# Performance work log

Measured on AMD Instinct MI355X. Metric: run time of the kernel, lower is better.

The kernel has to match this reference:

```python
import jax, jax.numpy as jnp
import numpy as np

VOCAB_SIZES = [100003, 100019, 100043, 100049, 100057, 100069, 100103, 100109,
               100129, 100151, 100153, 100169, 100183, 100189, 100193, 100207]
OFFSETS = np.cumsum([0] + VOCAB_SIZES[:-1]).astype(np.int32)  # per-head offsets into shared table
B, S, G, C = 2, 2048, 4, 2048        # batch, seq, hc_mult branches, base_emb_dim
H, DH = 16, 64                        # total hash heads, dim_per_head
ENGRAM_DIM = H * DH                   # 1024 = num_orders * dim_per_ngram
K, DIL = 4, 3                         # conv kernel_size, dilation = max_ngram_size


def setup_inputs() -> dict:
  key = jax.random.key(0)
  ks = jax.random.split(key, 8)
  total_vocab = sum(VOCAB_SIZES)
  return {
      "hidden_states": jax.random.normal(ks[0], (B, S, G, C), jnp.float32),
      "hash_input_ids": jax.random.randint(ks[1], (B, S, H), 0, min(VOCAB_SIZES), jnp.int32),
      "emb_table": jax.random.normal(ks[2], (total_vocab, DH), jnp.float32) * 0.02,
      "key_w": jax.random.normal(ks[3], (G, ENGRAM_DIM, C), jnp.float32) / np.sqrt(ENGRAM_DIM),
      "key_b": jnp.zeros((G, C), jnp.float32),
      "k_scale": jnp.ones((G, C), jnp.float32) + 0.02 * jax.random.normal(ks[4], (G, C), jnp.float32),
      "q_scale": jnp.ones((G, C), jnp.float32) + 0.02 * jax.random.normal(ks[5], (G, C), jnp.float32),
      "value_w": jax.random.normal(ks[6], (ENGRAM_DIM, C), jnp.float32) / np.sqrt(ENGRAM_DIM),
      "value_b": jnp.zeros((C,), jnp.float32),
      "conv_scale": jnp.ones((G, C), jnp.float32),
      "conv_w": jax.random.normal(ks[7], (K, G * C), jnp.float32) * 0.25,  # depthwise taps
  }


def _rmsnorm(x, scale, eps):
  var = jnp.mean(jnp.square(x), axis=-1, keepdims=True)
  return x * jax.lax.rsqrt(var + eps) * scale


def reference(hidden_states, hash_input_ids, emb_table, key_w, key_b,
              k_scale, q_scale, value_w, value_b, conv_scale, conv_w):
  # 1. Retrieve: offset-shifted multi-head embedding gather
  ids = hash_input_ids + jnp.asarray(OFFSETS)            # (B,S,H)
  emb = emb_table[ids].reshape(B, S, ENGRAM_DIM)         # (B,S,H*DH)
  # 2. Gate: per-branch key projections + RMSNorms, signed-sqrt sigmoid gate
  keys = jnp.einsum('bse,geo->bsgo', emb, key_w) + key_b  # (B,S,G,C)
  k = _rmsnorm(keys, k_scale, 1e-6)
  q = _rmsnorm(hidden_states, q_scale, 1e-6)
  qk = jnp.einsum('bsgc,bsgc->bsg', q, k) / jnp.sqrt(jnp.float32(C))
  gate_logits = jnp.sqrt(jnp.maximum(jnp.abs(qk), 1e-6)) * jnp.sign(qk)
  gates = jax.nn.sigmoid(gate_logits)                    # (B,S,G)
  value = emb @ value_w + value_b                        # (B,S,C)
  v = gates[..., None] * value[:, :, None, :]            # (B,S,G,C)
  # 3. Mix: ShortConv = SiLU(depthwise causal dilated Conv1D(RMSNorm(v)))
  xn = _rmsnorm(v, conv_scale, 1e-5).reshape(B, S, G * C)
  pad = (K - 1) * DIL                                    # causal left pad = 9
  xp = jnp.pad(xn, ((0, 0), (pad, 0), (0, 0)))
  y = sum(xp[:, j * DIL:j * DIL + S, :] * conv_w[j] for j in range(K))
  y = jax.nn.silu(y).reshape(B, S, G, C)
  return v + y
```

## Files before the change

### kernel.cpp

```cpp
#include <hip/hip_runtime.h>
#include <cstdint>
#include <cstddef>

typedef __attribute__((ext_vector_type(8))) __bf16 bf16x8;
typedef __attribute__((ext_vector_type(4))) float f32x4;
typedef __attribute__((ext_vector_type(4))) unsigned short u16x4;
typedef __attribute__((ext_vector_type(8))) unsigned short u16x8;

static constexpr int Bz = 2, Sz = 2048, Gz = 4, Cz = 2048;
static constexpr int Hh = 16, EDz = 1024;
static constexpr int Tz = Bz * Sz;
static constexpr int NALL = Gz * Cz + Cz;

__constant__ int OFF16[16] = {0, 100003, 200022, 300065, 400114, 500171, 600240,
                              700343, 800452, 900581, 1000732, 1100885, 1201054,
                              1301237, 1401426, 1501619};

__device__ __forceinline__ float bf2f(unsigned short s) {
  union { unsigned u; float f; } x; x.u = ((unsigned)s) << 16; return x.f;
}
__device__ __forceinline__ unsigned short f2bf(float f) {
  union { float f; unsigned u; } x; x.f = f;
  unsigned r = x.u + 0x7fff + ((x.u >> 16) & 1);
  return (unsigned short)(r >> 16);
}

__global__ __launch_bounds__(256) void k_prep0(float* __restrict__ sums) {
  int i = blockIdx.x * 256 + threadIdx.x;
  if (i < 53248) sums[i] = 0.f;
}

__global__ __launch_bounds__(256) void k_prepw(const float* __restrict__ key_w,
                                               const float* __restrict__ value_w,
                                               unsigned short* __restrict__ Wt) {
  __shared__ float tile[32][33];
  const int mat = blockIdx.y;
  const int ot = blockIdx.x & 63, kt = blockIdx.x >> 6;
  const float* src = (mat < 4) ? (key_w + (size_t)mat * EDz * Cz) : value_w;
  const int tx = threadIdx.x & 31, ty = threadIdx.x >> 5;
#pragma unroll
  for (int i = 0; i < 4; i++)
    tile[ty + i * 8][tx] = src[(size_t)(kt * 32 + ty + i * 8) * Cz + ot * 32 + tx];
  __syncthreads();
#pragma unroll
  for (int i = 0; i < 4; i++)
    Wt[(size_t)(mat * Cz + ot * 32 + ty + i * 8) * EDz + kt * 32 + tx] =
        f2bf(tile[tx][ty + i * 8]);
}

__global__ __launch_bounds__(256) void k_gather(const int* __restrict__ ids,
                                                const float* __restrict__ table,
                                                unsigned short* __restrict__ emb) {
  const int t = blockIdx.x;
  const int tid = threadIdx.x;
  const int h = tid >> 4;
  const int d = (tid & 15) * 4;
  const long row = (long)(ids[t * Hh + h] + OFF16[h]);
  f32x4 v = *reinterpret_cast<const f32x4*>(table + row * 64 + d);
  u16x4 o;
#pragma unroll
  for (int i = 0; i < 4; i++) o[i] = f2bf(v[i]);
  *reinterpret_cast<u16x4*>(emb + (size_t)t * EDz + tid * 4) = o;
}

#define GEMM_BAR  asm volatile("s_barrier" ::: "memory")
#define GEMM_V4   asm volatile("s_waitcnt vmcnt(4)" ::: "memory")

__global__ __launch_bounds__(512, 2) void k_gemm8f(const unsigned short* __restrict__ A,
                                                   const unsigned short* __restrict__ Bw,
                                                   const float* __restrict__ hidden,
                                                   const float* __restrict__ key_b,
                                                   const float* __restrict__ value_b,
                                                   const float* __restrict__ q_scale,
                                                   const float* __restrict__ k_scale,
                                                   float* __restrict__ sums,
                                                   unsigned short* __restrict__ vbuf) {
  __shared__ unsigned short s_lds[65536];
  char* lds_c = (char*)s_lds;

  const int tid = threadIdx.x;
  const int wid = tid >> 6, lane = tid & 63;
  const int wr = wid >> 2, wc = wid & 3;

  const int bid = blockIdx.x;
  const int swz = (bid & 7) * 80 + (bid >> 3);
  const int bm = swz / 40, bn = swz % 40;
  const int m0 = bm * 256, n0 = bn * 256;

  int rq[2], kq[2];
#pragma unroll
  for (int q = 0; q < 2; q++) {
    int x = q * 8192 + wid * 1024 + lane * 16;
    int y = x ^ (((x >> 9) & 1) << 5);
    rq[q] = ((y >> 11) & 7) * 16 + ((y >> 6) & 15);
    kq[q] = ((y >> 10) & 1) * 32 + ((y >> 1) & 31);
  }
  const int rdb = (((lane & 15) << 6) + ((lane >> 4) << 4)) ^ (((lane >> 3) & 1) << 5);

  const unsigned short* Arow0 = A + (size_t)m0 * EDz;
  const unsigned short* Arow1 = A + (size_t)(m0 + 128) * EDz;
  const unsigned short* Brow0 = Bw + (size_t)n0 * EDz;
  const unsigned short* Brow1 = Bw + (size_t)(n0 + 128) * EDz;

  auto STAGE = [&](const unsigned short* grow, int ldsOff, int kt) {
#pragma unroll
    for (int q = 0; q < 2; q++) {
      const unsigned short* src = grow + (size_t)rq[q] * EDz + kt * 64 + kq[q];
      __builtin_amdgcn_global_load_lds(
          (const __attribute__((address_space(1))) void*)src,
          (__attribute__((address_space(3))) void*)(lds_c + ldsOff + q * 8192 + wid * 1024),
          16, 0, 0);
    }
  };

  f32x4 acc[8][4] = {};
  bf16x8 Af[4][2], Bl[2][2], Bh[2][2];

  auto RD_A = [&](int buf, int msel) {
    const char* p = lds_c + buf * 32768 + wr * 16384 + rdb;
#pragma unroll
    for (int m = 0; m < 4; m++)
#pragma unroll
      for (int ks = 0; ks < 2; ks++)
        Af[m][ks] = *reinterpret_cast<const bf16x8*>(p + (msel * 4 + m) * 2048 + ks * 1024);
  };
  auto RD_B = [&](int buf, int nsel, bf16x8 (&Bf)[2][2]) {
    const char* p = lds_c + 65536 + buf * 32768 + (wc >> 1) * 16384 + (wc & 1) * 8192 + rdb;
#pragma unroll
    for (int n = 0; n < 2; n++)
#pragma unroll
      for (int ks = 0; ks < 2; ks++)
        Bf[n][ks] = *reinterpret_cast<const bf16x8*>(p + (nsel * 2 + n) * 2048 + ks * 1024);
  };
  auto MM = [&](int msel, int nsel, bf16x8 (&Bf)[2][2]) {
    __builtin_amdgcn_s_setprio(1);
#pragma unroll
    for (int m = 0; m < 4; m++)
#pragma unroll
      for (int n = 0; n < 2; n++)
#pragma unroll
        for (int ks = 0; ks < 2; ks++)
          acc[msel * 4 + m][nsel * 2 + n] = __builtin_amdgcn_mfma_f32_16x16x32_bf16(
              Af[m][ks], Bf[n][ks], acc[msel * 4 + m][nsel * 2 + n], 0, 0, 0);
    __builtin_amdgcn_s_setprio(0);
  };

  STAGE(Arow0, 0,             0);
  STAGE(Arow1, 16384,         0);
  STAGE(Brow0, 65536,         0);
  STAGE(Brow1, 65536 + 16384, 0);
  STAGE(Brow0, 65536 + 32768,         1);
  STAGE(Brow1, 65536 + 32768 + 16384, 1);
  GEMM_V4;
  GEMM_BAR;

  for (int i = 0; i < 8; ++i) {
    const int o  = 2 * i + 1;
    const int t2 = (2 * i + 2 > 15) ? 15 : 2 * i + 2;
    const int t3 = (2 * i + 3 > 15) ? 15 : 2 * i + 3;
    RD_A(0, 0); RD_B(0, 0, Bl);
    STAGE(Arow0, 32768, o);
    GEMM_BAR; MM(0, 0, Bl); GEMM_BAR;
    RD_B(0, 1, Bh);
    STAGE(Arow1, 32768 + 16384, o);
    GEMM_BAR; MM(0, 1, Bh); GEMM_BAR;
    RD_A(0, 1);
    STAGE(Brow0, 65536, t2);
    GEMM_BAR; MM(1, 0, Bl); GEMM_BAR;
    STAGE(Brow1, 65536 + 16384, t2);
    GEMM_V4;
    GEMM_BAR; MM(1, 1, Bh); GEMM_BAR;
    RD_A(1, 0); RD_B(1, 0, Bl);
    STAGE(Arow0, 0, t2);
    GEMM_BAR; MM(0, 0, Bl); GEMM_BAR;
    RD_B(1, 1, Bh);
    STAGE(Arow1, 16384, t2);
    GEMM_BAR; MM(0, 1, Bh); GEMM_BAR;
    RD_A(1, 1);
    STAGE(Brow0, 65536 + 32768, t3);
    GEMM_BAR; MM(1, 0, Bl); GEMM_BAR;
    STAGE(Brow1, 65536 + 32768 + 16384, t3);
    GEMM_V4;
    GEMM_BAR; MM(1, 1, Bh); GEMM_BAR;
  }

  float* sum_q2  = sums;
  float* sum_k2  = sums + 16384;
  float* sum_qwk = sums + 32768;
  float* sum_v2  = sums + 49152;

  if (n0 < 8192) {
    const int g = n0 >> 11;
#pragma unroll
    for (int mrep = 0; mrep < 8; mrep++) {
      const int rowb = wr * 128 + mrep * 16 + (lane >> 4) * 4;
#pragma unroll
      for (int nrep = 0; nrep < 4; nrep++) {
        const int coll = wc * 64 + nrep * 16 + (lane & 15);
        const float kb = key_b[n0 + coll];
#pragma unroll
        for (int t = 0; t < 4; t++) {
          const int row = rowb + t;
          const int addr = (row * 512 + coll * 2) ^ ((row & 15) << 4);
          *reinterpret_cast<unsigned short*>(lds_c + addr) =
              f2bf(acc[mrep][nrep][t] + kb);
        }
      }
    }
    __syncthreads();
    const int wrow = wid * 32;
    const int lrow = lane >> 3;
    const int lsub = lane & 7;
#pragma unroll
    for (int rr = 0; rr < 4; rr++) {
      const int row = wrow + rr * 8 + lrow;
      const int grow = m0 + row;
      const float* hp = hidden + (size_t)grow * 8192 + n0;
      float a_k2 = 0.f, a_qwk = 0.f, a_q2 = 0.f;
#pragma unroll
      for (int c8 = 0; c8 < 4; c8++) {
        const int lc = c8 * 64 + lsub * 8;
        const int addr = (row * 512 + lc * 2) ^ ((row & 15) << 4);
        bf16x8 k8 = *reinterpret_cast<const bf16x8*>(lds_c + addr);
        f32x4 h0 = *reinterpret_cast<const f32x4*>(hp + lc);
        f32x4 h1 = *reinterpret_cast<const f32x4*>(hp + lc + 4);
        f32x4 qs0 = *reinterpret_cast<const f32x4*>(q_scale + n0 + lc);
        f32x4 qs1 = *reinterpret_cast<const f32x4*>(q_scale + n0 + lc + 4);
        f32x4 ks0 = *reinterpret_cast<const f32x4*>(k_scale + n0 + lc);
        f32x4 ks1 = *reinterpret_cast<const f32x4*>(k_scale + n0 + lc + 4);
#pragma unroll
        for (int i = 0; i < 8; i++) {
          const float kf = (float)k8[i];
          const float hf = (i < 4) ? h0[i] : h1[i - 4];
          const float wf = ((i < 4) ? qs0[i] : qs1[i - 4]) *
                           ((i < 4) ? ks0[i] : ks1[i - 4]);
          a_k2  += kf * kf;
          a_qwk += kf * hf * wf;
          a_q2  += hf * hf;
        }
      }
#pragma unroll
      for (int msk = 1; msk <= 4; msk <<= 1) {
        a_k2  += __shfl_xor(a_k2, msk);
        a_qwk += __shfl_xor(a_qwk, msk);
        a_q2  += __shfl_xor(a_q2, msk);
      }
      if (lsub == 0) {
        const int idx = grow * 4 + g;
        atomicAdd(&sum_k2[idx], a_k2);
        atomicAdd(&sum_qwk[idx], a_qwk);
        atomicAdd(&sum_q2[idx], a_q2);
      }
    }
  } else {
#pragma unroll
    for (int mrep = 0; mrep < 8; mrep++) {
      const int rowb = m0 + wr * 128 + mrep * 16 + (lane >> 4) * 4;
      float av2[4] = {0.f, 0.f, 0.f, 0.f};
#pragma unroll
      for (int nrep = 0; nrep < 4; nrep++) {
        const int vcol = n0 - 8192 + wc * 64 + nrep * 16 + (lane & 15);
        const float vb = value_b[vcol];
#pragma unroll
        for (int t = 0; t < 4; t++) {
          const float v = acc[mrep][nrep][t] + vb;
          av2[t] += v * v;
          vbuf[(size_t)(rowb + t) * 2048 + vcol] = f2bf(v);
        }
      }
#pragma unroll
      for (int t = 0; t < 4; t++) {
        float a = av2[t];
#pragma unroll
        for (int msk = 1; msk <= 8; msk <<= 1) a += __shfl_xor(a, msk);
        if ((lane & 15) == 0) atomicAdd(&sum_v2[rowb + t], a);
      }
    }
  }
}

__global__ __launch_bounds__(256) void k_gatefin(const float* __restrict__ sums,
                                                 float* __restrict__ gates,
                                                 float* __restrict__ rstd) {
  const int i = blockIdx.x * 256 + threadIdx.x;
  const float* sum_q2  = sums;
  const float* sum_k2  = sums + 16384;
  const float* sum_qwk = sums + 32768;
  const float* sum_v2  = sums + 49152;
  const int t = i >> 2;
  const float invC = 1.f / 2048.f;
  const float inv_sqrtC = 0.02209708691f;
  float rqv = rsqrtf(sum_q2[i] * invC + 1e-6f);
  float rkv = rsqrtf(sum_k2[i] * invC + 1e-6f);
  float qk = sum_qwk[i] * rqv * rkv * inv_sqrtC;
  float l = sqrtf(fmaxf(fabsf(qk), 1e-6f));
  l = (qk < 0.f) ? -l : l;
  float gate = 1.f / (1.f + expf(-l));
  gates[i] = gate;
  rstd[i] = rsqrtf(gate * gate * (sum_v2[t] * invC) + 1e-5f);
}

__global__ __launch_bounds__(256) void k_conv(const unsigned short* __restrict__ vbuf,
                                              const float* __restrict__ gates,
                                              const float* __restrict__ rstd,
                                              const float* __restrict__ conv_scale,
                                              const float* __restrict__ conv_w,
                                              float* __restrict__ out) {
  const int th = threadIdx.x;
  const int r = blockIdx.x % 3, seg = blockIdx.x / 3;
  const int bg = blockIdx.y;
  const int b = bg >> 2, g = bg & 3;
  const int c8 = th * 8;
  const int ch = g * Cz + c8;

  float cs[8], w0[8], w1[8], w2[8], w3[8];
#pragma unroll
  for (int q = 0; q < 2; q++) {
    f32x4 a = *reinterpret_cast<const f32x4*>(conv_scale + ch + q * 4);
    f32x4 t0 = *reinterpret_cast<const f32x4*>(conv_w + 0 * 8192 + ch + q * 4);
    f32x4 t1 = *reinterpret_cast<const f32x4*>(conv_w + 1 * 8192 + ch + q * 4);
    f32x4 t2 = *reinterpret_cast<const f32x4*>(conv_w + 2 * 8192 + ch + q * 4);
    f32x4 t3 = *reinterpret_cast<const f32x4*>(conv_w + 3 * 8192 + ch + q * 4);
#pragma unroll
    for (int i = 0; i < 4; i++) {
      cs[q * 4 + i] = a[i];
      w0[q * 4 + i] = t0[i]; w1[q * 4 + i] = t1[i];
      w2[q * 4 + i] = t2[i]; w3[q * 4 + i] = t3[i];
    }
  }

  const int s_begin = seg * 64, s_end = s_begin + 64;
  const int s0 = s_begin + ((r - s_begin) % 3 + 3) % 3;

  float p1[8], p2[8], p3[8];
  auto ldxn = [&](int s, float* dst) {
    if (s < 0) {
#pragma unroll
      for (int i = 0; i < 8; i++) dst[i] = 0.f;
      return;
    }
    const int t = b * Sz + s;
    const float grs = gates[t * 4 + g] * rstd[t * 4 + g];
    u16x8 raw = *reinterpret_cast<const u16x8*>(vbuf + (size_t)t * 2048 + c8);
#pragma unroll
    for (int i = 0; i < 8; i++) dst[i] = bf2f(raw[i]) * grs * cs[i];
  };
  ldxn(s0 - 3, p1); ldxn(s0 - 6, p2); ldxn(s0 - 9, p3);

  for (int s = s0; s < s_end; s += 3) {
    const int t = b * Sz + s;
    const float gate = gates[t * 4 + g];
    const float rsc = rstd[t * 4 + g];
    u16x8 raw = *reinterpret_cast<const u16x8*>(vbuf + (size_t)t * 2048 + c8);
    f32x4 o0, o1;
#pragma unroll
    for (int i = 0; i < 8; i++) {
      float v = bf2f(raw[i]) * gate;
      float xn = v * rsc * cs[i];
      float y = w3[i] * xn + w2[i] * p1[i] + w1[i] * p2[i] + w0[i] * p3[i];
      float sy = y / (1.f + expf(-y));
      float ov = v + sy;
      if (i < 4) o0[i] = ov; else o1[i - 4] = ov;
      p3[i] = p2[i]; p2[i] = p1[i]; p1[i] = xn;
    }
    float* op = out + (size_t)t * (Gz * Cz) + ch;
    *reinterpret_cast<f32x4*>(op) = o0;
    *reinterpret_cast<f32x4*>(op + 4) = o1;
  }
}

extern "C" void kernel_launch(void* const* d_in, const int* in_sizes, int n_in,
                              void* d_out, int out_size, void* d_ws, size_t ws_size,
                              hipStream_t stream) {
  const float* hidden     = (const float*)d_in[0];
  const int*   hashids    = (const int*)d_in[1];
  const float* table      = (const float*)d_in[2];
  const float* key_w      = (const float*)d_in[3];
  const float* key_b      = (const float*)d_in[4];
  const float* k_scale    = (const float*)d_in[5];
  const float* q_scale    = (const float*)d_in[6];
  const float* value_w    = (const float*)d_in[7];
  const float* value_b    = (const float*)d_in[8];
  const float* conv_scale = (const float*)d_in[9];
  const float* conv_w     = (const float*)d_in[10];
  float* out = (float*)d_out;
  char* ws = (char*)d_ws;

  unsigned short* emb  = (unsigned short*)(ws + 0);
  unsigned short* Wt   = (unsigned short*)(ws + 8388608);
  unsigned short* vbuf = (unsigned short*)(ws + 29360128);
  float* sums  = (float*)(ws + 46137344);
  float* gates = (float*)(ws + 46350336);
  float* rstd  = (float*)(ws + 46415872);

  k_prep0<<<dim3(208), dim3(256), 0, stream>>>(sums);
  k_prepw<<<dim3(2048, 5), dim3(256), 0, stream>>>(key_w, value_w, Wt);
  k_gather<<<dim3(Tz), dim3(256), 0, stream>>>(hashids, table, emb);
  k_gemm8f<<<dim3(640), dim3(512), 0, stream>>>(emb, Wt, hidden, key_b, value_b,
                                                q_scale, k_scale, sums, vbuf);
  k_gatefin<<<dim3(64), dim3(256), 0, stream>>>(sums, gates, rstd);
  k_conv<<<dim3(96, 8), dim3(256), 0, stream>>>(vbuf, gates, rstd, conv_scale, conv_w, out);
}
```

Before: 202.0 us.

## Halve GEMM N-tile to 128 and double the grid

Shrinks the fused key/value GEMM block tile from 256x256 to 256x128. The B operand is now staged as a single 128-row slab with smaller LDS buffers, the pipeline schedule and vmcnt waits are reworked, and the epilogue swizzle is adjusted. The launch grid doubles to 1280 blocks, which gives finer wave granularity and a smaller tail, plus lower LDS and register pressure. In exchange, arithmetic intensity drops and A tiles are reloaded twice as often.

```diff
diff --git a/kernel.cpp b/kernel.cpp
--- a/kernel.cpp
+++ b/kernel.cpp
@@ -64,7 +64,7 @@
 }
 
 #define GEMM_BAR  asm volatile("s_barrier" ::: "memory")
-#define GEMM_V4   asm volatile("s_waitcnt vmcnt(4)" ::: "memory")
+#define GEMM_V2   asm volatile("s_waitcnt vmcnt(2)" ::: "memory")
 
 __global__ __launch_bounds__(512, 2) void k_gemm8f(const unsigned short* __restrict__ A,
                                                    const unsigned short* __restrict__ Bw,
@@ -75,7 +75,7 @@
                                                    const float* __restrict__ k_scale,
                                                    float* __restrict__ sums,
                                                    unsigned short* __restrict__ vbuf) {
-  __shared__ unsigned short s_lds[65536];
+  __shared__ unsigned short s_lds[49152];
   char* lds_c = (char*)s_lds;
 
   const int tid = threadIdx.x;
@@ -83,9 +83,9 @@
   const int wr = wid >> 2, wc = wid & 3;
 
   const int bid = blockIdx.x;
-  const int swz = (bid & 7) * 80 + (bid >> 3);
-  const int bm = swz / 40, bn = swz % 40;
-  const int m0 = bm * 256, n0 = bn * 256;
+  const int swz = (bid & 7) * 160 + (bid >> 3);
+  const int bm = swz / 80, bn = swz % 80;
+  const int m0 = bm * 256, n0 = bn * 128;
 
   int rq[2], kq[2];
 #pragma unroll
@@ -99,8 +99,7 @@
 
   const unsigned short* Arow0 = A + (size_t)m0 * EDz;
   const unsigned short* Arow1 = A + (size_t)(m0 + 128) * EDz;
-  const unsigned short* Brow0 = Bw + (size_t)n0 * EDz;
-  const unsigned short* Brow1 = Bw + (size_t)(n0 + 128) * EDz;
+  const unsigned short* Brow  = Bw + (size_t)n0 * EDz;
 
   auto STAGE = [&](const unsigned short* grow, int ldsOff, int kt) {
 #pragma unroll
@@ -113,8 +112,8 @@
     }
   };
 
-  f32x4 acc[8][4] = {};
-  bf16x8 Af[4][2], Bl[2][2], Bh[2][2];
+  f32x4 acc[8][2] = {};
+  bf16x8 Af[4][2], Bf[2][2];
 
   auto RD_A = [&](int buf, int msel) {
     const char* p = lds_c + buf * 32768 + wr * 16384 + rdb;
@@ -124,15 +123,15 @@
       for (int ks = 0; ks < 2; ks++)
         Af[m][ks] = *reinterpret_cast<const bf16x8*>(p + (msel * 4 + m) * 2048 + ks * 1024);
   };
-  auto RD_B = [&](int buf, int nsel, bf16x8 (&Bf)[2][2]) {
-    const char* p = lds_c + 65536 + buf * 32768 + (wc >> 1) * 16384 + (wc & 1) * 8192 + rdb;
+  auto RD_B = [&](int buf) {
+    const char* p = lds_c + 65536 + buf * 16384 + rdb;
 #pragma unroll
     for (int n = 0; n < 2; n++)
 #pragma unroll
       for (int ks = 0; ks < 2; ks++)
-        Bf[n][ks] = *reinterpret_cast<const bf16x8*>(p + (nsel * 2 + n) * 2048 + ks * 1024);
-  };
-  auto MM = [&](int msel, int nsel, bf16x8 (&Bf)[2][2]) {
+        Bf[n][ks] = *reinterpret_cast<const bf16x8*>(p + (wc * 2 + n) * 2048 + ks * 1024);
+  };
+  auto MM = [&](int msel) {
     __builtin_amdgcn_s_setprio(1);
 #pragma unroll
     for (int m = 0; m < 4; m++)
@@ -140,48 +139,38 @@
       for (int n = 0; n < 2; n++)
 #pragma unroll
         for (int ks = 0; ks < 2; ks++)
-          acc[msel * 4 + m][nsel * 2 + n] = __builtin_amdgcn_mfma_f32_16x16x32_bf16(
-              Af[m][ks], Bf[n][ks], acc[msel * 4 + m][nsel * 2 + n], 0, 0, 0);
+          acc[msel * 4 + m][n] = __builtin_amdgcn_mfma_f32_16x16x32_bf16(
+              Af[m][ks], Bf[n][ks], acc[msel * 4 + m][n], 0, 0, 0);
     __builtin_amdgcn_s_setprio(0);
   };
 
   STAGE(Arow0, 0,             0);
   STAGE(Arow1, 16384,         0);
-  STAGE(Brow0, 65536,         0);
-  STAGE(Brow1, 65536 + 16384, 0);
-  STAGE(Brow0, 65536 + 32768,         1);
-  STAGE(Brow1, 65536 + 32768 + 16384, 1);
-  GEMM_V4;
+  STAGE(Brow,  65536,         0);
+  STAGE(Brow,  65536 + 16384, 1);
+  GEMM_V2;
   GEMM_BAR;
 
   for (int i = 0; i < 8; ++i) {
     const int o  = 2 * i + 1;
     const int t2 = (2 * i + 2 > 15) ? 15 : 2 * i + 2;
     const int t3 = (2 * i + 3 > 15) ? 15 : 2 * i + 3;
-    RD_A(0, 0); RD_B(0, 0, Bl);
+    RD_A(0, 0); RD_B(0);
     STAGE(Arow0, 32768, o);
-    GEMM_BAR; MM(0, 0, Bl); GEMM_BAR;
-    RD_B(0, 1, Bh);
+    GEMM_BAR; MM(0); GEMM_BAR;
+    RD_A(0, 1);
     STAGE(Arow1, 32768 + 16384, o);
-    GEMM_BAR; MM(0, 1, Bh); GEMM_BAR;
-    RD_A(0, 1);
-    STAGE(Brow0, 65536, t2);
-    GEMM_BAR; MM(1, 0, Bl); GEMM_BAR;
-    STAGE(Brow1, 65536 + 16384, t2);
-    GEMM_V4;
-    GEMM_BAR; MM(1, 1, Bh); GEMM_BAR;
-    RD_A(1, 0); RD_B(1, 0, Bl);
+    STAGE(Brow,  65536, t2);
+    GEMM_V2;
+    GEMM_BAR; MM(1); GEMM_BAR;
+    RD_A(1, 0); RD_B(1);
     STAGE(Arow0, 0, t2);
-    GEMM_BAR; MM(0, 0, Bl); GEMM_BAR;
-    RD_B(1, 1, Bh);
+    GEMM_BAR; MM(0); GEMM_BAR;
+    RD_A(1, 1);
     STAGE(Arow1, 16384, t2);
-    GEMM_BAR; MM(0, 1, Bh); GEMM_BAR;
-    RD_A(1, 1);
-    STAGE(Brow0, 65536 + 32768, t3);
-    GEMM_BAR; MM(1, 0, Bl); GEMM_BAR;
-    STAGE(Brow1, 65536 + 32768 + 16384, t3);
-    GEMM_V4;
-    GEMM_BAR; MM(1, 1, Bh); GEMM_BAR;
+    STAGE(Brow,  65536 + 16384, t3);
+    GEMM_V2;
+    GEMM_BAR; MM(1); GEMM_BAR;
   }
 
   float* sum_q2  = sums;
@@ -195,13 +184,13 @@
     for (int mrep = 0; mrep < 8; mrep++) {
       const int rowb = wr * 128 + mrep * 16 + (lane >> 4) * 4;
 #pragma unroll
-      for (int nrep = 0; nrep < 4; nrep++) {
-        const int coll = wc * 64 + nrep * 16 + (lane & 15);
+      for (int nrep = 0; nrep < 2; nrep++) {
+        const int coll = wc * 32 + nrep * 16 + (lane & 15);
         const float kb = key_b[n0 + coll];
 #pragma unroll
         for (int t = 0; t < 4; t++) {
           const int row = rowb + t;
-          const int addr = (row * 512 + coll * 2) ^ ((row & 15) << 4);
+          const int addr = row * 256 + ((coll * 2) ^ ((row & 7) << 4));
           *reinterpret_cast<unsigned short*>(lds_c + addr) =
               f2bf(acc[mrep][nrep][t] + kb);
         }
@@ -218,9 +207,9 @@
       const float* hp = hidden + (size_t)grow * 8192 + n0;
       float a_k2 = 0.f, a_qwk = 0.f, a_q2 = 0.f;
 #pragma unroll
-      for (int c8 = 0; c8 < 4; c8++) {
+      for (int c8 = 0; c8 < 2; c8++) {
         const int lc = c8 * 64 + lsub * 8;
-        const int addr = (row * 512 + lc * 2) ^ ((row & 15) << 4);
+        const int addr = row * 256 + ((lc * 2) ^ ((row & 7) << 4));
         bf16x8 k8 = *reinterpret_cast<const bf16x8*>(lds_c + addr);
         f32x4 h0 = *reinterpret_cast<const f32x4*>(hp + lc);
         f32x4 h1 = *reinterpret_cast<const f32x4*>(hp + lc + 4);
@@ -258,8 +247,8 @@
       const int rowb = m0 + wr * 128 + mrep * 16 + (lane >> 4) * 4;
       float av2[4] = {0.f, 0.f, 0.f, 0.f};
 #pragma unroll
-      for (int nrep = 0; nrep < 4; nrep++) {
-        const int vcol = n0 - 8192 + wc * 64 + nrep * 16 + (lane & 15);
+      for (int nrep = 0; nrep < 2; nrep++) {
+        const int vcol = n0 - 8192 + wc * 32 + nrep * 16 + (lane & 15);
         const float vb = value_b[vcol];
 #pragma unroll
         for (int t = 0; t < 4; t++) {
@@ -396,8 +385,8 @@
   k_prep0<<<dim3(208), dim3(256), 0, stream>>>(sums);
   k_prepw<<<dim3(2048, 5), dim3(256), 0, stream>>>(key_w, value_w, Wt);
   k_gather<<<dim3(Tz), dim3(256), 0, stream>>>(hashids, table, emb);
-  k_gemm8f<<<dim3(640), dim3(512), 0, stream>>>(emb, Wt, hidden, key_b, value_b,
-                                                q_scale, k_scale, sums, vbuf);
+  k_gemm8f<<<dim3(1280), dim3(512), 0, stream>>>(emb, Wt, hidden, key_b, value_b,
+                                                 q_scale, k_scale, sums, vbuf);
   k_gatefin<<<dim3(64), dim3(256), 0, stream>>>(sums, gates, rstd);
   k_conv<<<dim3(96, 8), dim3(256), 0, stream>>>(vbuf, gates, rstd, conv_scale, conv_w, out);
 }
```

Measured after the change: 232.5 us. 15.1% more time.

## Split value GEMM into narrower 256x128 tiles to balance the block grid

Applied to the files above, without the earlier changes.

The fused key/value GEMM now uses 256x256 tiles only for the key columns (512 blocks). The value projection gets its own path with 256x128 tiles (256 blocks), which has a separate staging schedule, LDS layout and epilogue. This raises the grid from 640 to 768 blocks, aiming to improve wave quantization and load balance across CUs. In exchange the value tiles reuse less data per loaded A tile, and there is more code duplication and register variance between the two branches.

```diff
diff --git a/kernel.cpp b/kernel.cpp
--- a/kernel.cpp
+++ b/kernel.cpp
@@ -65,6 +65,7 @@
 
 #define GEMM_BAR  asm volatile("s_barrier" ::: "memory")
 #define GEMM_V4   asm volatile("s_waitcnt vmcnt(4)" ::: "memory")
+#define GEMM_V2   asm volatile("s_waitcnt vmcnt(2)" ::: "memory")
 
 __global__ __launch_bounds__(512, 2) void k_gemm8f(const unsigned short* __restrict__ A,
                                                    const unsigned short* __restrict__ Bw,
@@ -82,11 +83,6 @@
   const int wid = tid >> 6, lane = tid & 63;
   const int wr = wid >> 2, wc = wid & 3;
 
-  const int bid = blockIdx.x;
-  const int swz = (bid & 7) * 80 + (bid >> 3);
-  const int bm = swz / 40, bn = swz % 40;
-  const int m0 = bm * 256, n0 = bn * 256;
-
   int rq[2], kq[2];
 #pragma unroll
   for (int q = 0; q < 2; q++) {
@@ -97,99 +93,104 @@
   }
   const int rdb = (((lane & 15) << 6) + ((lane >> 4) << 4)) ^ (((lane >> 3) & 1) << 5);
 
-  const unsigned short* Arow0 = A + (size_t)m0 * EDz;
-  const unsigned short* Arow1 = A + (size_t)(m0 + 128) * EDz;
-  const unsigned short* Brow0 = Bw + (size_t)n0 * EDz;
-  const unsigned short* Brow1 = Bw + (size_t)(n0 + 128) * EDz;
-
-  auto STAGE = [&](const unsigned short* grow, int ldsOff, int kt) {
-#pragma unroll
-    for (int q = 0; q < 2; q++) {
-      const unsigned short* src = grow + (size_t)rq[q] * EDz + kt * 64 + kq[q];
-      __builtin_amdgcn_global_load_lds(
-          (const __attribute__((address_space(1))) void*)src,
-          (__attribute__((address_space(3))) void*)(lds_c + ldsOff + q * 8192 + wid * 1024),
-          16, 0, 0);
-    }
-  };
-
-  f32x4 acc[8][4] = {};
-  bf16x8 Af[4][2], Bl[2][2], Bh[2][2];
-
-  auto RD_A = [&](int buf, int msel) {
-    const char* p = lds_c + buf * 32768 + wr * 16384 + rdb;
-#pragma unroll
-    for (int m = 0; m < 4; m++)
-#pragma unroll
-      for (int ks = 0; ks < 2; ks++)
-        Af[m][ks] = *reinterpret_cast<const bf16x8*>(p + (msel * 4 + m) * 2048 + ks * 1024);
-  };
-  auto RD_B = [&](int buf, int nsel, bf16x8 (&Bf)[2][2]) {
-    const char* p = lds_c + 65536 + buf * 32768 + (wc >> 1) * 16384 + (wc & 1) * 8192 + rdb;
-#pragma unroll
-    for (int n = 0; n < 2; n++)
-#pragma unroll
-      for (int ks = 0; ks < 2; ks++)
-        Bf[n][ks] = *reinterpret_cast<const bf16x8*>(p + (nsel * 2 + n) * 2048 + ks * 1024);
-  };
-  auto MM = [&](int msel, int nsel, bf16x8 (&Bf)[2][2]) {
-    __builtin_amdgcn_s_setprio(1);
-#pragma unroll
-    for (int m = 0; m < 4; m++)
-#pragma unroll
-      for (int n = 0; n < 2; n++)
-#pragma unroll
-        for (int ks = 0; ks < 2; ks++)
-          acc[msel * 4 + m][nsel * 2 + n] = __builtin_amdgcn_mfma_f32_16x16x32_bf16(
-              Af[m][ks], Bf[n][ks], acc[msel * 4 + m][nsel * 2 + n], 0, 0, 0);
-    __builtin_amdgcn_s_setprio(0);
-  };
-
-  STAGE(Arow0, 0,             0);
-  STAGE(Arow1, 16384,         0);
-  STAGE(Brow0, 65536,         0);
-  STAGE(Brow1, 65536 + 16384, 0);
-  STAGE(Brow0, 65536 + 32768,         1);
-  STAGE(Brow1, 65536 + 32768 + 16384, 1);
-  GEMM_V4;
-  GEMM_BAR;
-
-  for (int i = 0; i < 8; ++i) {
-    const int o  = 2 * i + 1;
-    const int t2 = (2 * i + 2 > 15) ? 15 : 2 * i + 2;
-    const int t3 = (2 * i + 3 > 15) ? 15 : 2 * i + 3;
-    RD_A(0, 0); RD_B(0, 0, Bl);
-    STAGE(Arow0, 32768, o);
-    GEMM_BAR; MM(0, 0, Bl); GEMM_BAR;
-    RD_B(0, 1, Bh);
-    STAGE(Arow1, 32768 + 16384, o);
-    GEMM_BAR; MM(0, 1, Bh); GEMM_BAR;
-    RD_A(0, 1);
-    STAGE(Brow0, 65536, t2);
-    GEMM_BAR; MM(1, 0, Bl); GEMM_BAR;
-    STAGE(Brow1, 65536 + 16384, t2);
-    GEMM_V4;
-    GEMM_BAR; MM(1, 1, Bh); GEMM_BAR;
-    RD_A(1, 0); RD_B(1, 0, Bl);
-    STAGE(Arow0, 0, t2);
-    GEMM_BAR; MM(0, 0, Bl); GEMM_BAR;
-    RD_B(1, 1, Bh);
-    STAGE(Arow1, 16384, t2);
-    GEMM_BAR; MM(0, 1, Bh); GEMM_BAR;
-    RD_A(1, 1);
-    STAGE(Brow0, 65536 + 32768, t3);
-    GEMM_BAR; MM(1, 0, Bl); GEMM_BAR;
-    STAGE(Brow1, 65536 + 32768 + 16384, t3);
-    GEMM_V4;
-    GEMM_BAR; MM(1, 1, Bh); GEMM_BAR;
-  }
-
   float* sum_q2  = sums;
   float* sum_k2  = sums + 16384;
   float* sum_qwk = sums + 32768;
   float* sum_v2  = sums + 49152;
 
-  if (n0 < 8192) {
+  if (blockIdx.x < 512) {
+    const int bid = blockIdx.x;
+    const int swz = (bid & 7) * 64 + (bid >> 3);
+    const int bm = swz >> 5, bn = swz & 31;
+    const int m0 = bm * 256, n0 = bn * 256;
+
+    const unsigned short* Arow0 = A + (size_t)m0 * EDz;
+    const unsigned short* Arow1 = A + (size_t)(m0 + 128) * EDz;
+    const unsigned short* Brow0 = Bw + (size_t)n0 * EDz;
+    const unsigned short* Brow1 = Bw + (size_t)(n0 + 128) * EDz;
+
+    auto STAGE = [&](const unsigned short* grow, int ldsOff, int kt) {
+#pragma unroll
+      for (int q = 0; q < 2; q++) {
+        const unsigned short* src = grow + (size_t)rq[q] * EDz + kt * 64 + kq[q];
+        __builtin_amdgcn_global_load_lds(
+            (const __attribute__((address_space(1))) void*)src,
+            (__attribute__((address_space(3))) void*)(lds_c + ldsOff + q * 8192 + wid * 1024),
+            16, 0, 0);
+      }
+    };
+
+    f32x4 acc[8][4] = {};
+    bf16x8 Af[4][2], Bl[2][2], Bh[2][2];
+
+    auto RD_A = [&](int buf, int msel) {
+      const char* p = lds_c + buf * 32768 + wr * 16384 + rdb;
+#pragma unroll
+      for (int m = 0; m < 4; m++)
+#pragma unroll
+        for (int ks = 0; ks < 2; ks++)
+          Af[m][ks] = *reinterpret_cast<const bf16x8*>(p + (msel * 4 + m) * 2048 + ks * 1024);
+    };
+    auto RD_B = [&](int buf, int nsel, bf16x8 (&Bf)[2][2]) {
+      const char* p = lds_c + 65536 + buf * 32768 + (wc >> 1) * 16384 + (wc & 1) * 8192 + rdb;
+#pragma unroll
+      for (int n = 0; n < 2; n++)
+#pragma unroll
+        for (int ks = 0; ks < 2; ks++)
+          Bf[n][ks] = *reinterpret_cast<const bf16x8*>(p + (nsel * 2 + n) * 2048 + ks * 1024);
+    };
+    auto MM = [&](int msel, int nsel, bf16x8 (&Bf)[2][2]) {
+      __builtin_amdgcn_s_setprio(1);
+#pragma unroll
+      for (int m = 0; m < 4; m++)
+#pragma unroll
+        for (int n = 0; n < 2; n++)
+#pragma unroll
+          for (int ks = 0; ks < 2; ks++)
+            acc[msel * 4 + m][nsel * 2 + n] = __builtin_amdgcn_mfma_f32_16x16x32_bf16(
+                Af[m][ks], Bf[n][ks], acc[msel * 4 + m][nsel * 2 + n], 0, 0, 0);
+      __builtin_amdgcn_s_setprio(0);
+    };
+
+    STAGE(Arow0, 0,             0);
+    STAGE(Arow1, 16384,         0);
+    STAGE(Brow0, 65536,         0);
+    STAGE(Brow1, 65536 + 16384, 0);
+    STAGE(Brow0, 65536 + 32768,         1);
+    STAGE(Brow1, 65536 + 32768 + 16384, 1);
+    GEMM_V4;
+    GEMM_BAR;
+
+    for (int i = 0; i < 8; ++i) {
+      const int o  = 2 * i + 1;
+      const int t2 = (2 * i + 2 > 15) ? 15 : 2 * i + 2;
+      const int t3 = (2 * i + 3 > 15) ? 15 : 2 * i + 3;
+      RD_A(0, 0); RD_B(0, 0, Bl);
+      STAGE(Arow0, 32768, o);
+      GEMM_BAR; MM(0, 0, Bl); GEMM_BAR;
+      RD_B(0, 1, Bh);
+      STAGE(Arow1, 32768 + 16384, o);
+      GEMM_BAR; MM(0, 1, Bh); GEMM_BAR;
+      RD_A(0, 1);
+      STAGE(Brow0, 65536, t2);
+      GEMM_BAR; MM(1, 0, Bl); GEMM_BAR;
+      STAGE(Brow1, 65536 + 16384, t2);
+      GEMM_V4;
+      GEMM_BAR; MM(1, 1, Bh); GEMM_BAR;
+      RD_A(1, 0); RD_B(1, 0, Bl);
+      STAGE(Arow0, 0, t2);
+      GEMM_BAR; MM(0, 0, Bl); GEMM_BAR;
+      RD_B(1, 1, Bh);
+      STAGE(Arow1, 16384, t2);
+      GEMM_BAR; MM(0, 1, Bh); GEMM_BAR;
+      RD_A(1, 1);
+      STAGE(Brow0, 65536 + 32768, t3);
+      GEMM_BAR; MM(1, 0, Bl); GEMM_BAR;
+      STAGE(Brow1, 65536 + 32768 + 16384, t3);
+      GEMM_V4;
+      GEMM_BAR; MM(1, 1, Bh); GEMM_BAR;
+    }
+
     const int g = n0 >> 11;
 #pragma unroll
     for (int mrep = 0; mrep < 8; mrep++) {
@@ -253,17 +254,98 @@
       }
     }
   } else {
+    const int vb = blockIdx.x - 512;
+    const int swz = (vb & 7) * 32 + (vb >> 3);
+    const int bm = swz >> 4, bn = swz & 15;
+    const int m0 = bm * 256, n0v = bn * 128;
+
+    const unsigned short* Arow0 = A + (size_t)m0 * EDz;
+    const unsigned short* Arow1 = A + (size_t)(m0 + 128) * EDz;
+    const unsigned short* Brow  = Bw + (size_t)(8192 + n0v) * EDz;
+
+    auto STAGE = [&](const unsigned short* grow, int ldsOff, int kt) {
+#pragma unroll
+      for (int q = 0; q < 2; q++) {
+        const unsigned short* src = grow + (size_t)rq[q] * EDz + kt * 64 + kq[q];
+        __builtin_amdgcn_global_load_lds(
+            (const __attribute__((address_space(1))) void*)src,
+            (__attribute__((address_space(3))) void*)(lds_c + ldsOff + q * 8192 + wid * 1024),
+            16, 0, 0);
+      }
+    };
+
+    f32x4 acc[8][2] = {};
+    bf16x8 Af[4][2], Bf[2][2];
+
+    auto RD_A = [&](int buf, int msel) {
+      const char* p = lds_c + buf * 32768 + wr * 16384 + rdb;
+#pragma unroll
+      for (int m = 0; m < 4; m++)
+#pragma unroll
+        for (int ks = 0; ks < 2; ks++)
+          Af[m][ks] = *reinterpret_cast<const bf16x8*>(p + (msel * 4 + m) * 2048 + ks * 1024);
+    };
+    auto RD_B = [&](int buf) {
+      const char* p = lds_c + 65536 + buf * 16384 + rdb;
+#pragma unroll
+      for (int n = 0; n < 2; n++)
+#pragma unroll
+        for (int ks = 0; ks < 2; ks++)
+          Bf[n][ks] = *reinterpret_cast<const bf16x8*>(p + (wc * 2 + n) * 2048 + ks * 1024);
+    };
+    auto MM = [&](int msel) {
+      __builtin_amdgcn_s_setprio(1);
+#pragma unroll
+      for (int m = 0; m < 4; m++)
+#pragma unroll
+        for (int n = 0; n < 2; n++)
+#pragma unroll
+          for (int ks = 0; ks < 2; ks++)
+            acc[msel * 4 + m][n] = __builtin_amdgcn_mfma_f32_16x16x32_bf16(
+                Af[m][ks], Bf[n][ks], acc[msel * 4 + m][n], 0, 0, 0);
+      __builtin_amdgcn_s_setprio(0);
+    };
+
+    STAGE(Arow0, 0,             0);
+    STAGE(Arow1, 16384,         0);
+    STAGE(Brow,  65536,         0);
+    STAGE(Brow,  65536 + 16384, 1);
+    GEMM_V2;
+    GEMM_BAR;
+
+    for (int i = 0; i < 8; ++i) {
+      const int o  = 2 * i + 1;
+      const int t2 = (2 * i + 2 > 15) ? 15 : 2 * i + 2;
+      const int t3 = (2 * i + 3 > 15) ? 15 : 2 * i + 3;
+      RD_A(0, 0); RD_B(0);
+      STAGE(Arow0, 32768, o);
+      GEMM_BAR; MM(0); GEMM_BAR;
+      RD_A(0, 1);
+      STAGE(Arow1, 32768 + 16384, o);
+      STAGE(Brow,  65536, t2);
+      GEMM_V2;
+      GEMM_BAR; MM(1); GEMM_BAR;
+      RD_A(1, 0); RD_B(1);
+      STAGE(Arow0, 0, t2);
+      GEMM_BAR; MM(0); GEMM_BAR;
+      RD_A(1, 1);
+      STAGE(Arow1, 16384, t2);
+      STAGE(Brow,  65536 + 16384, t3);
+      GEMM_V2;
+      GEMM_BAR; MM(1); GEMM_BAR;
+    }
+
 #pragma unroll
     for (int mrep = 0; mrep < 8; mrep++) {
       const int rowb = m0 + wr * 128 + mrep * 16 + (lane >> 4) * 4;
       float av2[4] = {0.f, 0.f, 0.f, 0.f};
 #pragma unroll
-      for (int nrep = 0; nrep < 4; nrep++) {
-        const int vcol = n0 - 8192 + wc * 64 + nrep * 16 + (lane & 15);
-        const float vb = value_b[vcol];
+      for (int nrep = 0; nrep < 2; nrep++) {
+        const int vcol = n0v + wc * 32 + nrep * 16 + (lane & 15);
+        const float vb2 = value_b[vcol];
 #pragma unroll
         for (int t = 0; t < 4; t++) {
-          const float v = acc[mrep][nrep][t] + vb;
+          const float v = acc[mrep][nrep][t] + vb2;
           av2[t] += v * v;
           vbuf[(size_t)(rowb + t) * 2048 + vcol] = f2bf(v);
         }
@@ -396,7 +478,7 @@
   k_prep0<<<dim3(208), dim3(256), 0, stream>>>(sums);
   k_prepw<<<dim3(2048, 5), dim3(256), 0, stream>>>(key_w, value_w, Wt);
   k_gather<<<dim3(Tz), dim3(256), 0, stream>>>(hashids, table, emb);
-  k_gemm8f<<<dim3(640), dim3(512), 0, stream>>>(emb, Wt, hidden, key_b, value_b,
+  k_gemm8f<<<dim3(768), dim3(512), 0, stream>>>(emb, Wt, hidden, key_b, value_b,
                                                 q_scale, k_scale, sums, vbuf);
   k_gatefin<<<dim3(64), dim3(256), 0, stream>>>(sums, gates, rstd);
   k_conv<<<dim3(96, 8), dim3(256), 0, stream>>>(vbuf, gates, rstd, conv_scale, conv_w, out);
```

New measurement: 209.6 us. +3.8%, slower.

## Rewrite fused GEMM as 1024-thread blocks with K=32 double-buffered tiles

Applied to the files above, without the earlier changes.

Replaces the 512-thread, 8-phase interleaved GEMM (K-step 64, 128 KB LDS) with a 1024-thread block where each of 16 waves computes a 64x64 subtile. The new loop double-buffers K=32 tiles in 64 KB of LDS, waiting on vmcnt(0) with one barrier per step. The key epilogue now runs in two halves so it fits the smaller LDS. The goal is more waves per CU and lower register pressure, at the cost of the finer-grained load/MFMA interleave, more barriers, and full waits on global loads each step.

```diff
diff --git a/kernel.cpp b/kernel.cpp
--- a/kernel.cpp
+++ b/kernel.cpp
@@ -64,18 +64,18 @@
 }
 
 #define GEMM_BAR  asm volatile("s_barrier" ::: "memory")
-#define GEMM_V4   asm volatile("s_waitcnt vmcnt(4)" ::: "memory")
-
-__global__ __launch_bounds__(512, 2) void k_gemm8f(const unsigned short* __restrict__ A,
-                                                   const unsigned short* __restrict__ Bw,
-                                                   const float* __restrict__ hidden,
-                                                   const float* __restrict__ key_b,
-                                                   const float* __restrict__ value_b,
-                                                   const float* __restrict__ q_scale,
-                                                   const float* __restrict__ k_scale,
-                                                   float* __restrict__ sums,
-                                                   unsigned short* __restrict__ vbuf) {
-  __shared__ unsigned short s_lds[65536];
+#define GEMM_V0   asm volatile("s_waitcnt vmcnt(0)" ::: "memory")
+
+__global__ __launch_bounds__(1024, 4) void k_gemm1k(const unsigned short* __restrict__ A,
+                                                    const unsigned short* __restrict__ Bw,
+                                                    const float* __restrict__ hidden,
+                                                    const float* __restrict__ key_b,
+                                                    const float* __restrict__ value_b,
+                                                    const float* __restrict__ q_scale,
+                                                    const float* __restrict__ k_scale,
+                                                    float* __restrict__ sums,
+                                                    unsigned short* __restrict__ vbuf) {
+  __shared__ unsigned short s_lds[32768];
   char* lds_c = (char*)s_lds;
 
   const int tid = threadIdx.x;
@@ -87,101 +87,53 @@
   const int bm = swz / 40, bn = swz % 40;
   const int m0 = bm * 256, n0 = bn * 256;
 
-  int rq[2], kq[2];
-#pragma unroll
-  for (int q = 0; q < 2; q++) {
-    int x = q * 8192 + wid * 1024 + lane * 16;
-    int y = x ^ (((x >> 9) & 1) << 5);
-    rq[q] = ((y >> 11) & 7) * 16 + ((y >> 6) & 15);
-    kq[q] = ((y >> 10) & 1) * 32 + ((y >> 1) & 31);
-  }
-  const int rdb = (((lane & 15) << 6) + ((lane >> 4) << 4)) ^ (((lane >> 3) & 1) << 5);
-
-  const unsigned short* Arow0 = A + (size_t)m0 * EDz;
-  const unsigned short* Arow1 = A + (size_t)(m0 + 128) * EDz;
-  const unsigned short* Brow0 = Bw + (size_t)n0 * EDz;
-  const unsigned short* Brow1 = Bw + (size_t)(n0 + 128) * EDz;
+  const unsigned short* Arow = A + (size_t)m0 * EDz;
+  const unsigned short* Brow = Bw + (size_t)n0 * EDz;
+  const int srow = wid * 16 + (lane >> 2);
+  const int scol = (lane & 3) * 8;
 
   auto STAGE = [&](const unsigned short* grow, int ldsOff, int kt) {
-#pragma unroll
-    for (int q = 0; q < 2; q++) {
-      const unsigned short* src = grow + (size_t)rq[q] * EDz + kt * 64 + kq[q];
-      __builtin_amdgcn_global_load_lds(
-          (const __attribute__((address_space(1))) void*)src,
-          (__attribute__((address_space(3))) void*)(lds_c + ldsOff + q * 8192 + wid * 1024),
-          16, 0, 0);
-    }
+    const unsigned short* src = grow + (size_t)srow * EDz + kt * 32 + scol;
+    __builtin_amdgcn_global_load_lds(
+        (const __attribute__((address_space(1))) void*)src,
+        (__attribute__((address_space(3))) void*)(lds_c + ldsOff + wid * 1024),
+        16, 0, 0);
   };
 
-  f32x4 acc[8][4] = {};
-  bf16x8 Af[4][2], Bl[2][2], Bh[2][2];
-
-  auto RD_A = [&](int buf, int msel) {
-    const char* p = lds_c + buf * 32768 + wr * 16384 + rdb;
+  f32x4 acc[4][4] = {};
+  bf16x8 Af[4], Bf[4];
+  const int ar = wr * 64, br = wc * 64;
+  const int lr15 = lane & 15;
+  const int kb = (lane >> 4) * 16;
+
+  STAGE(Arow, 0, 0);
+  STAGE(Brow, 32768, 0);
+  GEMM_V0;
+  GEMM_BAR;
+
+  for (int t = 0; t < 32; ++t) {
+    const int cur = (t & 1) * 16384;
+    if (t < 31) {
+      STAGE(Arow, 16384 - cur, t + 1);
+      STAGE(Brow, 32768 + (16384 - cur), t + 1);
+    }
+    const char* pa = lds_c + cur;
+    const char* pb = lds_c + 32768 + cur;
 #pragma unroll
     for (int m = 0; m < 4; m++)
-#pragma unroll
-      for (int ks = 0; ks < 2; ks++)
-        Af[m][ks] = *reinterpret_cast<const bf16x8*>(p + (msel * 4 + m) * 2048 + ks * 1024);
-  };
-  auto RD_B = [&](int buf, int nsel, bf16x8 (&Bf)[2][2]) {
-    const char* p = lds_c + 65536 + buf * 32768 + (wc >> 1) * 16384 + (wc & 1) * 8192 + rdb;
-#pragma unroll
-    for (int n = 0; n < 2; n++)
-#pragma unroll
-      for (int ks = 0; ks < 2; ks++)
-        Bf[n][ks] = *reinterpret_cast<const bf16x8*>(p + (nsel * 2 + n) * 2048 + ks * 1024);
-  };
-  auto MM = [&](int msel, int nsel, bf16x8 (&Bf)[2][2]) {
+      Af[m] = *reinterpret_cast<const bf16x8*>(pa + (ar + m * 16 + lr15) * 64 + kb);
+#pragma unroll
+    for (int n = 0; n < 4; n++)
+      Bf[n] = *reinterpret_cast<const bf16x8*>(pb + (br + n * 16 + lr15) * 64 + kb);
     __builtin_amdgcn_s_setprio(1);
 #pragma unroll
     for (int m = 0; m < 4; m++)
 #pragma unroll
-      for (int n = 0; n < 2; n++)
-#pragma unroll
-        for (int ks = 0; ks < 2; ks++)
-          acc[msel * 4 + m][nsel * 2 + n] = __builtin_amdgcn_mfma_f32_16x16x32_bf16(
-              Af[m][ks], Bf[n][ks], acc[msel * 4 + m][nsel * 2 + n], 0, 0, 0);
+      for (int n = 0; n < 4; n++)
+        acc[m][n] = __builtin_amdgcn_mfma_f32_16x16x32_bf16(Af[m], Bf[n], acc[m][n], 0, 0, 0);
     __builtin_amdgcn_s_setprio(0);
-  };
-
-  STAGE(Arow0, 0,             0);
-  STAGE(Arow1, 16384,         0);
-  STAGE(Brow0, 65536,         0);
-  STAGE(Brow1, 65536 + 16384, 0);
-  STAGE(Brow0, 65536 + 32768,         1);
-  STAGE(Brow1, 65536 + 32768 + 16384, 1);
-  GEMM_V4;
-  GEMM_BAR;
-
-  for (int i = 0; i < 8; ++i) {
-    const int o  = 2 * i + 1;
-    const int t2 = (2 * i + 2 > 15) ? 15 : 2 * i + 2;
-    const int t3 = (2 * i + 3 > 15) ? 15 : 2 * i + 3;
-    RD_A(0, 0); RD_B(0, 0, Bl);
-    STAGE(Arow0, 32768, o);
-    GEMM_BAR; MM(0, 0, Bl); GEMM_BAR;
-    RD_B(0, 1, Bh);
-    STAGE(Arow1, 32768 + 16384, o);
-    GEMM_BAR; MM(0, 1, Bh); GEMM_BAR;
-    RD_A(0, 1);
-    STAGE(Brow0, 65536, t2);
-    GEMM_BAR; MM(1, 0, Bl); GEMM_BAR;
-    STAGE(Brow1, 65536 + 16384, t2);
-    GEMM_V4;
-    GEMM_BAR; MM(1, 1, Bh); GEMM_BAR;
-    RD_A(1, 0); RD_B(1, 0, Bl);
-    STAGE(Arow0, 0, t2);
-    GEMM_BAR; MM(0, 0, Bl); GEMM_BAR;
-    RD_B(1, 1, Bh);
-    STAGE(Arow1, 16384, t2);
-    GEMM_BAR; MM(0, 1, Bh); GEMM_BAR;
-    RD_A(1, 1);
-    STAGE(Brow0, 65536 + 32768, t3);
-    GEMM_BAR; MM(1, 0, Bl); GEMM_BAR;
-    STAGE(Brow1, 65536 + 32768 + 16384, t3);
-    GEMM_V4;
-    GEMM_BAR; MM(1, 1, Bh); GEMM_BAR;
+    GEMM_V0;
+    GEMM_BAR;
   }
 
   float* sum_q2  = sums;
@@ -192,35 +144,36 @@
   if (n0 < 8192) {
     const int g = n0 >> 11;
 #pragma unroll
-    for (int mrep = 0; mrep < 8; mrep++) {
-      const int rowb = wr * 128 + mrep * 16 + (lane >> 4) * 4;
-#pragma unroll
-      for (int nrep = 0; nrep < 4; nrep++) {
-        const int coll = wc * 64 + nrep * 16 + (lane & 15);
-        const float kb = key_b[n0 + coll];
-#pragma unroll
-        for (int t = 0; t < 4; t++) {
-          const int row = rowb + t;
-          const int addr = (row * 512 + coll * 2) ^ ((row & 15) << 4);
-          *reinterpret_cast<unsigned short*>(lds_c + addr) =
-              f2bf(acc[mrep][nrep][t] + kb);
+    for (int p = 0; p < 2; p++) {
+      if (p) __syncthreads();
+      if ((wr >> 1) == p) {
+#pragma unroll
+        for (int mrep = 0; mrep < 4; mrep++) {
+          const int lrb = (wr & 1) * 64 + mrep * 16 + (lane >> 4) * 4;
+#pragma unroll
+          for (int nrep = 0; nrep < 4; nrep++) {
+            const int coll = wc * 64 + nrep * 16 + lr15;
+            const float kbv = key_b[n0 + coll];
+#pragma unroll
+            for (int t2 = 0; t2 < 4; t2++) {
+              const int lr = lrb + t2;
+              const int addr = lr * 512 + ((coll * 2) ^ ((lr & 15) << 4));
+              *reinterpret_cast<unsigned short*>(lds_c + addr) =
+                  f2bf(acc[mrep][nrep][t2] + kbv);
+            }
+          }
         }
       }
-    }
-    __syncthreads();
-    const int wrow = wid * 32;
-    const int lrow = lane >> 3;
-    const int lsub = lane & 7;
-#pragma unroll
-    for (int rr = 0; rr < 4; rr++) {
-      const int row = wrow + rr * 8 + lrow;
-      const int grow = m0 + row;
+      __syncthreads();
+      const int lr = wid * 8 + (lane >> 3);
+      const int lsub = lane & 7;
+      const int grow = m0 + p * 128 + lr;
       const float* hp = hidden + (size_t)grow * 8192 + n0;
       float a_k2 = 0.f, a_qwk = 0.f, a_q2 = 0.f;
 #pragma unroll
       for (int c8 = 0; c8 < 4; c8++) {
         const int lc = c8 * 64 + lsub * 8;
-        const int addr = (row * 512 + lc * 2) ^ ((row & 15) << 4);
+        const int addr = lr * 512 + ((lc * 2) ^ ((lr & 15) << 4));
         bf16x8 k8 = *reinterpret_cast<const bf16x8*>(lds_c + addr);
         f32x4 h0 = *reinterpret_cast<const f32x4*>(hp + lc);
         f32x4 h1 = *reinterpret_cast<const f32x4*>(hp + lc + 4);
@@ -254,26 +207,26 @@
     }
   } else {
 #pragma unroll
-    for (int mrep = 0; mrep < 8; mrep++) {
-      const int rowb = m0 + wr * 128 + mrep * 16 + (lane >> 4) * 4;
+    for (int mrep = 0; mrep < 4; mrep++) {
+      const int rowb = m0 + wr * 64 + mrep * 16 + (lane >> 4) * 4;
       float av2[4] = {0.f, 0.f, 0.f, 0.f};
 #pragma unroll
       for (int nrep = 0; nrep < 4; nrep++) {
-        const int vcol = n0 - 8192 + wc * 64 + nrep * 16 + (lane & 15);
-        const float vb = value_b[vcol];
-#pragma unroll
-        for (int t = 0; t < 4; t++) {
-          const float v = acc[mrep][nrep][t] + vb;
-          av2[t] += v * v;
-          vbuf[(size_t)(rowb + t) * 2048 + vcol] = f2bf(v);
+        const int vcol = n0 - 8192 + wc * 64 + nrep * 16 + lr15;
+        const float vb2 = value_b[vcol];
+#pragma unroll
+        for (int t2 = 0; t2 < 4; t2++) {
+          const float v = acc[mrep][nrep][t2] + vb2;
+          av2[t2] += v * v;
+          vbuf[(size_t)(rowb + t2) * 2048 + vcol] = f2bf(v);
         }
       }
 #pragma unroll
-      for (int t = 0; t < 4; t++) {
-        float a = av2[t];
+      for (int t2 = 0; t2 < 4; t2++) {
+        float a = av2[t2];
 #pragma unroll
         for (int msk = 1; msk <= 8; msk <<= 1) a += __shfl_xor(a, msk);
-        if ((lane & 15) == 0) atomicAdd(&sum_v2[rowb + t], a);
+        if (lr15 == 0) atomicAdd(&sum_v2[rowb + t2], a);
       }
     }
   }
@@ -396,8 +349,8 @@
   k_prep0<<<dim3(208), dim3(256), 0, stream>>>(sums);
   k_prepw<<<dim3(2048, 5), dim3(256), 0, stream>>>(key_w, value_w, Wt);
   k_gather<<<dim3(Tz), dim3(256), 0, stream>>>(hashids, table, emb);
-  k_gemm8f<<<dim3(640), dim3(512), 0, stream>>>(emb, Wt, hidden, key_b, value_b,
-                                                q_scale, k_scale, sums, vbuf);
+  k_gemm1k<<<dim3(640), dim3(1024), 0, stream>>>(emb, Wt, hidden, key_b, value_b,
+                                                 q_scale, k_scale, sums, vbuf);
   k_gatefin<<<dim3(64), dim3(256), 0, stream>>>(sums, gates, rstd);
   k_conv<<<dim3(96, 8), dim3(256), 0, stream>>>(vbuf, gates, rstd, conv_scale, conv_w, out);
 }
```

After: 211.9 us. +4.9%, slower.
